# Performance work log

Measured on AMD Instinct MI355X. Metric: run time of the kernel, lower is better.

## Reference

```python
import jax, jax.numpy as jnp
import numpy as np

N_NODES = 100000
N_EDGES = 1200000
MAX_ATOM_TYPE = 100
NUM_FEATURES = 92
GC_DIM = 64          # pre_layer_dim == gc_dim == CGConv channels
NUM_RBF = 32
NUM_GC_LAYERS = 4
CUTOFF_UPPER = 5.0
BN_EPS = 1e-5


def setup_inputs() -> dict:
    key = jax.random.key(0)
    ks = jax.random.split(key, 12)
    atom_types = jax.random.randint(ks[0], (N_NODES,), 0, MAX_ATOM_TYPE, dtype=jnp.int32)
    pos = jax.random.uniform(ks[1], (N_NODES, 3), dtype=jnp.float32) * 6.0  # box side 6 -> many dists < cutoff
    edge_index = jax.random.randint(ks[2], (2, N_EDGES), 0, N_NODES, dtype=jnp.int32)
    # parameters
    emb = jax.random.normal(ks[3], (MAX_ATOM_TYPE, NUM_FEATURES), dtype=jnp.float32)
    s = 1.0 / np.sqrt(NUM_FEATURES)
    pre_W = jax.random.uniform(ks[4], (NUM_FEATURES, GC_DIM), minval=-s, maxval=s, dtype=jnp.float32)
    pre_b = jnp.zeros((GC_DIM,), jnp.float32)
    zdim = 2 * GC_DIM + NUM_RBF  # [x_i, x_j, edge_attr]
    sz = 1.0 / np.sqrt(zdim)
    Wf = jax.random.uniform(ks[5], (NUM_GC_LAYERS, zdim, GC_DIM), minval=-sz, maxval=sz, dtype=jnp.float32)
    bf = jnp.zeros((NUM_GC_LAYERS, GC_DIM), jnp.float32)
    Ws = jax.random.uniform(ks[6], (NUM_GC_LAYERS, zdim, GC_DIM), minval=-sz, maxval=sz, dtype=jnp.float32)
    bs = jnp.zeros((NUM_GC_LAYERS, GC_DIM), jnp.float32)
    bn_gamma = jnp.ones((NUM_GC_LAYERS, GC_DIM), jnp.float32)
    bn_beta = jnp.zeros((NUM_GC_LAYERS, GC_DIM), jnp.float32)
    # ExpNormalSmearing (torchmd-net) init
    start = np.exp(-CUTOFF_UPPER)
    means = jnp.asarray(np.linspace(start, 1.0, NUM_RBF), jnp.float32)
    betas = jnp.full((NUM_RBF,), (2.0 / NUM_RBF * (1.0 - start)) ** -2, jnp.float32)
    return {"atom_types": atom_types, "pos": pos, "edge_index": edge_index,
            "emb": emb, "pre_W": pre_W, "pre_b": pre_b,
            "Wf": Wf, "bf": bf, "Ws": Ws, "bs": bs,
            "bn_gamma": bn_gamma, "bn_beta": bn_beta,
            "means": means, "betas": betas}


def _forward(atom_types, pos, edge_index, emb, pre_W, pre_b, Wf, bf, Ws, bs,
             bn_gamma, bn_beta, means, betas):
    src, dst = edge_index[0], edge_index[1]
    # distance (edge_vec = pos[src] - pos[dst])
    vec = pos[src] - pos[dst]                                  # [E,3]
    dist = jnp.sqrt(jnp.sum(vec * vec, axis=-1) + 1e-12)       # [E]
    # expnorm RBF with cosine cutoff (cutoff_lower = 0)
    cutoff = 0.5 * (jnp.cos(dist * (np.pi / CUTOFF_UPPER)) + 1.0) * (dist < CUTOFF_UPPER)
    alpha = 5.0 / CUTOFF_UPPER
    edge_attr = cutoff[:, None] * jnp.exp(
        -betas * (jnp.exp(-alpha * dist)[:, None] - means) ** 2)  # [E,NUM_RBF]
    # embedding + pre layer
    x = emb[atom_types]                                        # [N,F]
    x = jax.nn.relu(x @ pre_W + pre_b)                         # [N,C]
    # mean-aggregation degree (scatter-mean denominator)
    deg = jax.ops.segment_sum(jnp.ones_like(dist), dst, num_segments=N_NODES)
    inv_deg = jnp.where(deg > 0, 1.0 / jnp.maximum(deg, 1.0), 0.0)[:, None]
    for l in range(NUM_GC_LAYERS):
        # CGConv: z = [x_i, x_j, e]; out = x + mean_j(sigmoid(lin_f(z)) * softplus(lin_s(z)))
        z = jnp.concatenate([x[dst], x[src], edge_attr], axis=-1)   # [E, 2C+R]
        msg = jax.nn.sigmoid(z @ Wf[l] + bf[l]) * jax.nn.softplus(z @ Ws[l] + bs[l])
        agg = jax.ops.segment_sum(msg, dst, num_segments=N_NODES) * inv_deg
        x = x + agg
        # BatchNorm1d (batch statistics, biased var, as in torch training mode)
        mu = jnp.mean(x, axis=0)
        var = jnp.mean((x - mu) ** 2, axis=0)
        x = (x - mu) * jax.lax.rsqrt(var + BN_EPS) * bn_gamma[l] + bn_beta[l]
    return x


def reference(atom_types, pos, edge_index, emb, pre_W, pre_b, Wf, bf, Ws, bs,
              bn_gamma, bn_beta, means, betas):
    return _forward(atom_types, pos, edge_index, emb, pre_W, pre_b, Wf, bf, Ws, bs,
                    bn_gamma, bn_beta, means, betas)
```

## Files before the change

### kernel.cpp

```cpp
#include <hip/hip_runtime.h>
#include <math.h>

#define N_NODES 100000
#define N_EDGES 1200000
#define GC 64
#define RBF 32
#define NLAYERS 4
#define NF 92
#define NATOM 100
#define BN_EPS 1e-5f
#define TILE_GRID 2048
#define NWIN (N_EDGES / 16)
#define LOG2E 1.44269504f
#define LN2 0.69314718f

typedef _Float16 half8 __attribute__((ext_vector_type(8)));
typedef _Float16 half4 __attribute__((ext_vector_type(4)));
typedef _Float16 half2v __attribute__((ext_vector_type(2)));
typedef float f32x4 __attribute__((ext_vector_type(4)));
union U32H2 { unsigned int u; half2v h; };

__global__ __launch_bounds__(256) void deg_kernel(
    const int* __restrict__ ei, int* __restrict__ deg)
{
    int e = blockIdx.x * 256 + threadIdx.x;
    if (e >= N_EDGES) return;
    atomicAdd(&deg[ei[N_EDGES + e]], 1);
}

__global__ __launch_bounds__(256) void scan_a_kernel(const int* __restrict__ deg, int* __restrict__ bsums)
{
    __shared__ int sm[256];
    int tid = threadIdx.x;
    int i = blockIdx.x * 256 + tid;
    int v = (i < N_NODES) ? deg[i] : 0;
    sm[tid] = v;
    __syncthreads();
    for (int s = 128; s > 0; s >>= 1) {
        if (tid < s) sm[tid] += sm[tid + s];
        __syncthreads();
    }
    if (tid == 0) bsums[blockIdx.x] = sm[0];
}

__global__ __launch_bounds__(512) void scan_b_kernel(const int* __restrict__ bsums, int* __restrict__ boffs)
{
    __shared__ int sm[512];
    int tid = threadIdx.x;
    int v = (tid < 391) ? bsums[tid] : 0;
    sm[tid] = v;
    __syncthreads();
    for (int off = 1; off < 512; off <<= 1) {
        int t = (tid >= off) ? sm[tid - off] : 0;
        __syncthreads();
        sm[tid] += t;
        __syncthreads();
    }
    boffs[tid] = (tid == 0) ? 0 : sm[tid - 1];
}

__global__ __launch_bounds__(256) void scan_c_kernel(
    const int* __restrict__ deg, const int* __restrict__ boffs,
    int* __restrict__ row_st, float* __restrict__ inv_deg)
{
    __shared__ int sm[256];
    int tid = threadIdx.x;
    int i = blockIdx.x * 256 + tid;
    int v = (i < N_NODES) ? deg[i] : 0;
    sm[tid] = v;
    __syncthreads();
    for (int off = 1; off < 256; off <<= 1) {
        int t = (tid >= off) ? sm[tid - off] : 0;
        __syncthreads();
        sm[tid] += t;
        __syncthreads();
    }
    if (i <= N_NODES) row_st[i] = boffs[blockIdx.x] + sm[tid] - v;
    if (i < N_NODES) inv_deg[i] = (v > 0) ? (1.0f / (float)v) : 0.0f;
}

__global__ __launch_bounds__(256) void scatter_perm_kernel(
    const int* __restrict__ ei, const int* __restrict__ row_st,
    int* __restrict__ cursor, int2* __restrict__ csr_sd)
{
    int e = blockIdx.x * 256 + threadIdx.x;
    if (e >= N_EDGES) return;
    int s = ei[e];
    int d = ei[N_EDGES + e];
    int p = atomicAdd(&cursor[d], 1);
    csr_sd[row_st[d] + p] = make_int2(s, d);
}

__global__ __launch_bounds__(256) void edge_post_kernel(
    const int2* __restrict__ csr_sd, const float* __restrict__ pos,
    const float* __restrict__ inv_deg,
    const float* __restrict__ means, const float* __restrict__ betas,
    int* __restrict__ csr_src, int* __restrict__ csr_dst,
    unsigned int* __restrict__ ea,
    unsigned char* __restrict__ seg8, int* __restrict__ wnode,
    _Float16* __restrict__ inv_e)
{
    __shared__ int sdst[256];
    int t = blockIdx.x * 256 + threadIdx.x;
    if (t < N_EDGES) {
        int2 v = csr_sd[t];
        int s = v.x, d = v.y;
        csr_src[t] = s;
        csr_dst[t] = d;
        sdst[threadIdx.x] = d;
        inv_e[t] = (_Float16)(inv_deg[d] * LN2);

        float dx = pos[s * 3 + 0] - pos[d * 3 + 0];
        float dy = pos[s * 3 + 1] - pos[d * 3 + 1];
        float dz = pos[s * 3 + 2] - pos[d * 3 + 2];
        float dist = sqrtf(dx * dx + dy * dy + dz * dz + 1e-12f);
        float cut = 0.0f;
        if (dist < 5.0f) cut = 0.5f * (__cosf(dist * 0.6283185307179586f) + 1.0f);
        float ex = __expf(-dist);
        union { _Float16 h[32]; uint4 u[4]; } pk;
#pragma unroll
        for (int k = 0; k < 32; k++) {
            float vk = ex - means[k];
            pk.h[k] = (_Float16)(cut * __expf(-betas[k] * vk * vk));
        }
        uint4* op = (uint4*)(ea + (size_t)t * 16);
        op[0] = pk.u[0];
        op[1] = pk.u[1];
        op[2] = pk.u[2];
        op[3] = pk.u[3];
    }
    __syncthreads();
    if (threadIdx.x < 16) {
        int w0 = blockIdx.x * 16 + threadIdx.x;
        if ((size_t)w0 * 16 < N_EDGES) {
            int lb = threadIdx.x * 16;
            int gb = w0 * 16;
            int prev = -1, sg = -1;
            for (int k = 0; k < 16; k++) {
                int dd = sdst[lb + k];
                if (dd != prev) { sg++; prev = dd; wnode[gb + sg] = dd; }
                seg8[gb + k] = (unsigned char)sg;
            }
            for (int m = sg + 1; m < 16; m++) wnode[gb + m] = -1;
        }
    }
}

__global__ __launch_bounds__(256) void prep_const_kernel(
    const float* __restrict__ Wf, const float* __restrict__ Ws,
    _Float16* __restrict__ wf16, _Float16* __restrict__ ws16,
    const float* __restrict__ emb, const float* __restrict__ pre_W,
    const float* __restrict__ pre_b, float* __restrict__ T)
{
    int b = blockIdx.x;
    if (b < 160) {
        int i = b * 256 + threadIdx.x;
        int l = i / (160 * GC);
        int r = i - l * 160 * GC;
        int k = r >> 6;
        int col = r & 63;
        size_t o = ((size_t)l * GC + col) * 160 + k;
        wf16[o] = (_Float16)(Wf[i] * LOG2E);
        ws16[o] = (_Float16)(Ws[i] * LOG2E);
    } else {
        int a = (b - 160) * 4 + (threadIdx.x >> 6);
        int c = threadIdx.x & 63;
        if (a < NATOM) {
            float acc = pre_b[c];
            for (int k = 0; k < NF; k++) acc = fmaf(emb[a * NF + k], pre_W[k * GC + c], acc);
            T[a * GC + c] = fmaxf(acc, 0.0f);
        }
    }
}

__global__ __launch_bounds__(256) void xinit_kernel(
    const int* __restrict__ atom_types, const float* __restrict__ T,
    float* __restrict__ x, _Float16* __restrict__ x16)
{
    int i = blockIdx.x * 256 + threadIdx.x;
    int n = i >> 4;
    int a = atom_types[n];
    float4 v = ((const float4*)T)[a * 16 + (i & 15)];
    ((float4*)x)[i] = v;
    half4 h = { (_Float16)v.x, (_Float16)v.y, (_Float16)v.z, (_Float16)v.w };
    ((half4*)x16)[i] = h;
}

static __device__ __forceinline__ void proj_mfma16(
    const _Float16* __restrict__ wf, const _Float16* __restrict__ ws,
    const float* __restrict__ bfv, const float* __restrict__ bsv,
    const half8 Bn[2], int cb, int node, unsigned int* __restrict__ P2u)
{
    const int lane = threadIdx.x & 63;
    const int quad = lane >> 4;
    const int r16 = lane & 15;
    f32x4 accf[2], accs[2];
#pragma unroll
    for (int sub = 0; sub < 2; sub++) {
        accf[sub] = (f32x4){0.f, 0.f, 0.f, 0.f};
        accs[sub] = (f32x4){0.f, 0.f, 0.f, 0.f};
    }
#pragma unroll
    for (int kt = 0; kt < 2; kt++) {
#pragma unroll
        for (int sub = 0; sub < 2; sub++) {
            int chan = cb + sub * 16 + r16;
            half8 a = *(const half8*)(wf + (size_t)chan * 160 + kt * 32 + quad * 8);
            half8 b = *(const half8*)(ws + (size_t)chan * 160 + kt * 32 + quad * 8);
            accf[sub] = __builtin_amdgcn_mfma_f32_16x16x32_f16(a, Bn[kt], accf[sub], 0, 0, 0);
            accs[sub] = __builtin_amdgcn_mfma_f32_16x16x32_f16(b, Bn[kt], accs[sub], 0, 0, 0);
        }
    }
#pragma unroll
    for (int sub = 0; sub < 2; sub++) {
        float4 bf4 = *(const float4*)(bfv + cb + sub * 16 + quad * 4);
        float4 bs4 = *(const float4*)(bsv + cb + sub * 16 + quad * 4);
        half8 h = { (_Float16)(accf[sub][0] + bf4.x * LOG2E), (_Float16)(accs[sub][0] + bs4.x * LOG2E),
                    (_Float16)(accf[sub][1] + bf4.y * LOG2E), (_Float16)(accs[sub][1] + bs4.y * LOG2E),
                    (_Float16)(accf[sub][2] + bf4.z * LOG2E), (_Float16)(accs[sub][2] + bs4.z * LOG2E),
                    (_Float16)(accf[sub][3] + bf4.w * LOG2E), (_Float16)(accs[sub][3] + bs4.w * LOG2E) };
        *(half8*)(P2u + (size_t)node * GC + cb + sub * 16 + quad * 4) = h;
    }
}

__global__ __launch_bounds__(256) void proj_kernel(
    const _Float16* __restrict__ x16,
    const _Float16* __restrict__ wf, const _Float16* __restrict__ ws,
    const float* __restrict__ bfv, const float* __restrict__ bsv,
    unsigned int* __restrict__ P2u)
{
    const int lane = threadIdx.x & 63;
    const int wid = threadIdx.x >> 6;
    const int quad = lane >> 4;
    const int r16 = lane & 15;
    const int wgid = blockIdx.x * 4 + wid;
    const int cb = (wgid & 1) * 32;
    const int nb = (wgid >> 1) * 16;
    half8 Bn[2];
    Bn[0] = *(const half8*)(x16 + (size_t)(nb + r16) * GC + quad * 8);
    Bn[1] = *(const half8*)(x16 + (size_t)(nb + r16) * GC + 32 + quad * 8);
    proj_mfma16(wf, ws, bfv, bsv, Bn, cb, nb + r16, P2u);
}

__global__ __launch_bounds__(256) void bnproj_kernel(
    const float* __restrict__ xn, const float* __restrict__ stats,
    const float* __restrict__ gamma, const float* __restrict__ beta,
    float* __restrict__ xout, _Float16* __restrict__ x16,
    const _Float16* __restrict__ wf, const _Float16* __restrict__ ws,
    const float* __restrict__ bfv, const float* __restrict__ bsv,
    unsigned int* __restrict__ P2u)
{
    __shared__ _Float16 lx[32 * 72];
    const int nb = blockIdx.x * 32;
    const float invN = 1.0f / (float)N_NODES;

#pragma unroll
    for (int rep = 0; rep < 2; rep++) {
        int g = rep * 256 + threadIdx.x;
        int gi = blockIdx.x * 512 + g;
        int node = g >> 4;
        int c4 = (g & 15) * 4;
        float4 v = ((const float4*)xn)[gi];
        float vv[4] = {v.x, v.y, v.z, v.w};
        float o[4];
#pragma unroll
        for (int t = 0; t < 4; t++) {
            int c = c4 + t;
            float mu = stats[c] * invN;
            float var = stats[64 + c] * invN - mu * mu;
            float sc = gamma[c] * rsqrtf(var + BN_EPS);
            o[t] = (vv[t] - mu) * sc + beta[c];
        }
        ((float4*)xout)[gi] = make_float4(o[0], o[1], o[2], o[3]);
        half4 h = { (_Float16)o[0], (_Float16)o[1], (_Float16)o[2], (_Float16)o[3] };
        ((half4*)x16)[gi] = h;
        *(half4*)(lx + node * 72 + c4) = h;
    }
    __syncthreads();

    const int lane = threadIdx.x & 63;
    const int wid = threadIdx.x >> 6;
    const int quad = lane >> 4;
    const int r16 = lane & 15;
    const int cb = (wid & 1) * 32;
    const int tn = (wid >> 1) * 16 + r16;
    half8 Bn[2];
    Bn[0] = *(const half8*)(lx + tn * 72 + quad * 8);
    Bn[1] = *(const half8*)(lx + tn * 72 + 32 + quad * 8);
    proj_mfma16(wf, ws, bfv, bsv, Bn, cb, nb + tn, P2u);
}

static __device__ __forceinline__ void compute_win(
    half8 S0, half8 S1, half8 E, int4 d4, int moff,
    const half8 (&WGF)[3][2], const half8 (&WGS)[3][2],
    int r16, int quad, int cb,
    const unsigned char* __restrict__ seg8, const int* __restrict__ wnode,
    const _Float16* __restrict__ inv_e, const unsigned int* __restrict__ P2u,
    float* __restrict__ x)
{
    unsigned int pv0, pv1, pv2, pv3, pv4, pv5, pv6, pv7;
    {
        const unsigned int* p0 = P2u + (size_t)d4.x * GC + cb + r16;
        const unsigned int* p1 = P2u + (size_t)d4.y * GC + cb + r16;
        const unsigned int* p2 = P2u + (size_t)d4.z * GC + cb + r16;
        const unsigned int* p3 = P2u + (size_t)d4.w * GC + cb + r16;
        pv0 = p0[0];  pv4 = p0[16];
        pv1 = p1[0];  pv5 = p1[16];
        pv2 = p2[0];  pv6 = p2[16];
        pv3 = p3[0];  pv7 = p3[16];
    }
    unsigned int segq = *(const unsigned int*)(seg8 + moff + quad * 4);
    int4 wn4 = *(const int4*)(wnode + moff + quad * 4);
    half4 inv4 = *(const half4*)(inv_e + moff + quad * 4);

    const f32x4 zf = (f32x4){0.0f, 0.0f, 0.0f, 0.0f};
    f32x4 accf[2], accs[2];
    __builtin_amdgcn_s_setprio(1);
#pragma unroll
    for (int ctl = 0; ctl < 2; ctl++) {
        accf[ctl] = __builtin_amdgcn_mfma_f32_16x16x32_f16(S0, WGF[0][ctl], zf, 0, 0, 0);
        accs[ctl] = __builtin_amdgcn_mfma_f32_16x16x32_f16(S0, WGS[0][ctl], zf, 0, 0, 0);
        accf[ctl] = __builtin_amdgcn_mfma_f32_16x16x32_f16(S1, WGF[1][ctl], accf[ctl], 0, 0, 0);
        accs[ctl] = __builtin_amdgcn_mfma_f32_16x16x32_f16(S1, WGS[1][ctl], accs[ctl], 0, 0, 0);
        accf[ctl] = __builtin_amdgcn_mfma_f32_16x16x32_f16(E,  WGF[2][ctl], accf[ctl], 0, 0, 0);
        accs[ctl] = __builtin_amdgcn_mfma_f32_16x16x32_f16(E,  WGS[2][ctl], accs[ctl], 0, 0, 0);
    }
    __builtin_amdgcn_s_setprio(0);

    unsigned int pvv[8] = {pv0, pv1, pv2, pv3, pv4, pv5, pv6, pv7};
    half4 msgh[2];
#pragma unroll
    for (int ctl = 0; ctl < 2; ctl++) {
#pragma unroll
        for (int rr = 0; rr < 4; rr++) {
            U32H2 t; t.u = pvv[ctl * 4 + rr];
            float af = accf[ctl][rr] + (float)t.h.x;
            float as = accs[ctl][rr] + (float)t.h.y;
            float sg = __builtin_amdgcn_rcpf(1.0f + __builtin_amdgcn_exp2f(-af));
            float sp = __builtin_amdgcn_logf(1.0f + __builtin_amdgcn_exp2f(as));
            msgh[ctl][rr] = (_Float16)(sg * sp);
        }
    }
    half4 am;
#pragma unroll
    for (int j = 0; j < 4; j++) {
        int sj = (segq >> (8 * j)) & 0xff;
        am[j] = (sj == r16) ? inv4[j] : (_Float16)0.0f;
    }
    int wa[4] = { wn4.x, wn4.y, wn4.z, wn4.w };
#pragma unroll
    for (int ctl = 0; ctl < 2; ctl++) {
        f32x4 red = __builtin_amdgcn_mfma_f32_16x16x16f16(am, msgh[ctl], zf, 0, 0, 0);
#pragma unroll
        for (int rr = 0; rr < 4; rr++) {
            int nd = wa[rr];
            if (nd >= 0) atomicAdd(&x[(size_t)nd * GC + cb + ctl * 16 + r16], red[rr]);
        }
    }
}

#define LOADSET(S0_, S1_, EE_, SRC_, WW_)                                            \
    S0_ = *(const half8*)(x16 + (size_t)(SRC_) * GC + quad * 8);                     \
    S1_ = *(const half8*)(x16 + (size_t)(SRC_) * GC + 32 + quad * 8);                \
    EE_ = *(const half8*)(ea + ((size_t)(WW_) * 16 + r16) * RBF + quad * 8);

__global__ __launch_bounds__(256, 3) void win_mfma_kernel(
    const _Float16* __restrict__ x16, const _Float16* __restrict__ ea,
    const int* __restrict__ csr_src, const int* __restrict__ csr_dst,
    const unsigned char* __restrict__ seg8, const int* __restrict__ wnode,
    const _Float16* __restrict__ inv_e, const unsigned int* __restrict__ P2u,
    const _Float16* __restrict__ wf16, const _Float16* __restrict__ ws16,
    float* __restrict__ x)
{
    const int lane = threadIdx.x & 63;
    const int wid = __builtin_amdgcn_readfirstlane(threadIdx.x >> 6);
    const int quad = lane >> 4;
    const int r16 = lane & 15;
    const int wgid = blockIdx.x * 4 + wid;
    const int cb = (wgid & 1) * 32;
    int w = wgid >> 1;
    const int NSEQ = TILE_GRID * 2;

    half8 WGF[3][2], WGS[3][2];
#pragma unroll
    for (int ctl = 0; ctl < 2; ctl++) {
        const _Float16* wfp = wf16 + (size_t)(cb + ctl * 16 + r16) * 160 + 64 + quad * 8;
        const _Float16* wsp = ws16 + (size_t)(cb + ctl * 16 + r16) * 160 + 64 + quad * 8;
#pragma unroll
        for (int kt = 0; kt < 3; kt++) {
            WGF[kt][ctl] = *(const half8*)(wfp + kt * 32);
            WGS[kt][ctl] = *(const half8*)(wsp + kt * 32);
        }
    }

    int sA = csr_src[w * 16 + r16];
    int4 d4A = *(const int4*)(csr_dst + w * 16 + quad * 4);
    half8 AS0, AS1, AE;
    LOADSET(AS0, AS1, AE, sA, w);
    int moffA = w * 16;

    int wB = w + NSEQ; if (wB >= NWIN) wB = NWIN - 1;
    int sB = csr_src[wB * 16 + r16];
    int4 d4B = *(const int4*)(csr_dst + wB * 16 + quad * 4);
    half8 BS0, BS1, BE;
    LOADSET(BS0, BS1, BE, sB, wB);
    int moffB = wB * 16;

    int wC = wB + NSEQ; if (wC >= NWIN) wC = NWIN - 1;
    int sC = csr_src[wC * 16 + r16];
    int4 d4C = *(const int4*)(csr_dst + wC * 16 + quad * 4);

    while (true) {
        compute_win(AS0, AS1, AE, d4A, moffA,
                    WGF, WGS, r16, quad, cb, seg8, wnode, inv_e, P2u, x);
        LOADSET(AS0, AS1, AE, sC, wC);
        d4A = d4C; moffA = wC * 16;
        wC += NSEQ; if (wC >= NWIN) wC = NWIN - 1;
        sC = csr_src[wC * 16 + r16];
        d4C = *(const int4*)(csr_dst + wC * 16 + quad * 4);
        w += NSEQ;
        if (w >= NWIN) break;

        compute_win(BS0, BS1, BE, d4B, moffB,
                    WGF, WGS, r16, quad, cb, seg8, wnode, inv_e, P2u, x);
        LOADSET(BS0, BS1, BE, sC, wC);
        d4B = d4C; moffB = wC * 16;
        wC += NSEQ; if (wC >= NWIN) wC = NWIN - 1;
        sC = csr_src[wC * 16 + r16];
        d4C = *(const int4*)(csr_dst + wC * 16 + quad * 4);
        w += NSEQ;
        if (w >= NWIN) break;
    }
}

__global__ __launch_bounds__(256) void stats_kernel(const float* __restrict__ x, float* __restrict__ stats)
{
    const int lane = threadIdx.x & 63;
    const int wid = threadIdx.x >> 6;
    int w = blockIdx.x * 4 + wid;
    float s1 = 0.0f, s2 = 0.0f;
    for (int n = w; n < N_NODES; n += 2048) {
        float v = x[(size_t)n * GC + lane];
        s1 += v;
        s2 = fmaf(v, v, s2);
    }
    __shared__ float rs1[4][64];
    __shared__ float rs2[4][64];
    rs1[wid][lane] = s1;
    rs2[wid][lane] = s2;
    __syncthreads();
    if (threadIdx.x < 64) {
        atomicAdd(&stats[lane], rs1[0][lane] + rs1[1][lane] + rs1[2][lane] + rs1[3][lane]);
    } else if (threadIdx.x < 128) {
        int c = threadIdx.x & 63;
        atomicAdd(&stats[64 + c], rs2[0][c] + rs2[1][c] + rs2[2][c] + rs2[3][c]);
    }
}

__global__ __launch_bounds__(256) void bn_kernel(
    const float* __restrict__ xn, const float* __restrict__ stats,
    const float* __restrict__ gamma, const float* __restrict__ beta,
    float* __restrict__ out)
{
    int i = blockIdx.x * 256 + threadIdx.x;
    int c4 = (i & 15) * 4;
    float4 v = ((const float4*)xn)[i];
    float vv[4] = {v.x, v.y, v.z, v.w};
    float o[4];
    const float invN = 1.0f / (float)N_NODES;
#pragma unroll
    for (int t = 0; t < 4; t++) {
        int c = c4 + t;
        float mu = stats[c] * invN;
        float var = stats[64 + c] * invN - mu * mu;
        float sc = gamma[c] * rsqrtf(var + BN_EPS);
        o[t] = (vv[t] - mu) * sc + beta[c];
    }
    ((float4*)out)[i] = make_float4(o[0], o[1], o[2], o[3]);
}

extern "C" void kernel_launch(void* const* d_in, const int* in_sizes, int n_in,
                              void* d_out, int out_size, void* d_ws, size_t ws_size,
                              hipStream_t stream)
{
    const int* atom_types = (const int*)d_in[0];
    const float* pos = (const float*)d_in[1];
    const int* edge_index = (const int*)d_in[2];
    const float* emb = (const float*)d_in[3];
    const float* pre_W = (const float*)d_in[4];
    const float* pre_b = (const float*)d_in[5];
    const float* Wf = (const float*)d_in[6];
    const float* bf = (const float*)d_in[7];
    const float* Ws = (const float*)d_in[8];
    const float* bs = (const float*)d_in[9];
    const float* gamma = (const float*)d_in[10];
    const float* beta = (const float*)d_in[11];
    const float* means = (const float*)d_in[12];
    const float* betas = (const float*)d_in[13];

    char* base = (char*)d_ws;
    char* p = base;
    auto alloc = [&](size_t bytes) -> char* {
        char* r = p;
        p += (bytes + 255) & ~(size_t)255;
        return r;
    };
    unsigned int* ea = (unsigned int*)alloc((size_t)N_EDGES * RBF * 2);
    float* x = (float*)alloc((size_t)N_NODES * GC * 4);
    _Float16* x16 = (_Float16*)alloc((size_t)N_NODES * GC * 2);
    unsigned int* P2u = (unsigned int*)alloc((size_t)N_NODES * GC * 4);
    int2* csr_sd = (int2*)alloc((size_t)N_EDGES * 8);
    int* csr_src = (int*)alloc((size_t)N_EDGES * 4);
    int* csr_dst = (int*)alloc((size_t)N_EDGES * 4);
    int* wnode = (int*)alloc((size_t)N_EDGES * 4);
    unsigned char* seg8 = (unsigned char*)alloc((size_t)N_EDGES);
    _Float16* inv_e = (_Float16*)alloc((size_t)N_EDGES * 2);
    _Float16* wf16 = (_Float16*)alloc((size_t)NLAYERS * GC * 160 * 2);
    _Float16* ws16 = (_Float16*)alloc((size_t)NLAYERS * GC * 160 * 2);
    int* row_st = (int*)alloc((size_t)(N_NODES + 1) * 4);
    float* inv_deg = (float*)alloc((size_t)N_NODES * 4);
    float* T = (float*)alloc((size_t)NATOM * GC * 4);
    int* bsums = (int*)alloc(512 * 4);
    int* boffs = (int*)alloc(512 * 4);
    const size_t ZR_INTS = (size_t)2 * N_NODES + 128 * NLAYERS + 64;
    char* zr = alloc(ZR_INTS * 4);
    int* deg = (int*)zr;
    int* cursor = deg + N_NODES;
    float* stats = (float*)(cursor + N_NODES);

    if ((size_t)(p - base) > ws_size) return;

    (void)hipMemsetAsync(zr, 0, ZR_INTS * 4, stream);

    const int EG = (N_EDGES + 255) / 256;
    deg_kernel<<<EG, 256, 0, stream>>>(edge_index, deg);
    scan_a_kernel<<<391, 256, 0, stream>>>(deg, bsums);
    scan_b_kernel<<<1, 512, 0, stream>>>(bsums, boffs);
    scan_c_kernel<<<391, 256, 0, stream>>>(deg, boffs, row_st, inv_deg);
    scatter_perm_kernel<<<EG, 256, 0, stream>>>(edge_index, row_st, cursor, csr_sd);
    edge_post_kernel<<<EG, 256, 0, stream>>>(csr_sd, pos, inv_deg, means, betas,
                                             csr_src, csr_dst, ea, seg8, wnode, inv_e);
    prep_const_kernel<<<185, 256, 0, stream>>>(Wf, Ws, wf16, ws16, emb, pre_W, pre_b, T);
    xinit_kernel<<<N_NODES * 16 / 256, 256, 0, stream>>>(atom_types, T, x, x16);
    proj_kernel<<<N_NODES / 32, 256, 0, stream>>>(x16, wf16, ws16, bf, bs, P2u);

    for (int l = 0; l < NLAYERS; l++) {
        win_mfma_kernel<<<TILE_GRID, 256, 0, stream>>>(
            x16, (const _Float16*)ea, csr_src, csr_dst, seg8, wnode, inv_e, P2u,
            wf16 + (size_t)l * GC * 160, ws16 + (size_t)l * GC * 160, x);
        stats_kernel<<<512, 256, 0, stream>>>(x, stats + l * 128);
        if (l < NLAYERS - 1) {
            bnproj_kernel<<<N_NODES / 32, 256, 0, stream>>>(
                x, stats + l * 128, gamma + l * GC, beta + l * GC, x, x16,
                wf16 + (size_t)(l + 1) * GC * 160, ws16 + (size_t)(l + 1) * GC * 160,
                bf + (l + 1) * GC, bs + (l + 1) * GC, P2u);
        } else {
            bn_kernel<<<N_NODES * 16 / 256, 256, 0, stream>>>(
                x, stats + l * 128, gamma + l * GC, beta + l * GC, (float*)d_out);
        }
    }
}
```

Baseline: 816.4 us.

## Deepen edge-window prefetch to three buffers and fuse init with projection

The windowed message kernel now keeps three windows of gathered operands in flight instead of two, so global-memory gathers for later windows overlap more compute. Separately, the embedding-lookup init kernel is fused into the first projection kernel through shared memory, removing one launch and a round trip of x16 through global memory. The deeper prefetch raises register pressure, which may lower occupancy or cause spills.

```diff
diff --git a/kernel.cpp b/kernel.cpp
--- a/kernel.cpp
+++ b/kernel.cpp
@@ -173,19 +173,6 @@
     }
 }
 
-__global__ __launch_bounds__(256) void xinit_kernel(
-    const int* __restrict__ atom_types, const float* __restrict__ T,
-    float* __restrict__ x, _Float16* __restrict__ x16)
-{
-    int i = blockIdx.x * 256 + threadIdx.x;
-    int n = i >> 4;
-    int a = atom_types[n];
-    float4 v = ((const float4*)T)[a * 16 + (i & 15)];
-    ((float4*)x)[i] = v;
-    half4 h = { (_Float16)v.x, (_Float16)v.y, (_Float16)v.z, (_Float16)v.w };
-    ((half4*)x16)[i] = h;
-}
-
 static __device__ __forceinline__ void proj_mfma16(
     const _Float16* __restrict__ wf, const _Float16* __restrict__ ws,
     const float* __restrict__ bfv, const float* __restrict__ bsv,
@@ -223,36 +210,15 @@
     }
 }
 
-__global__ __launch_bounds__(256) void proj_kernel(
-    const _Float16* __restrict__ x16,
+__global__ __launch_bounds__(256) void initproj_kernel(
+    const int* __restrict__ atom_types, const float* __restrict__ T,
+    float* __restrict__ x, _Float16* __restrict__ x16,
     const _Float16* __restrict__ wf, const _Float16* __restrict__ ws,
     const float* __restrict__ bfv, const float* __restrict__ bsv,
     unsigned int* __restrict__ P2u)
 {
-    const int lane = threadIdx.x & 63;
-    const int wid = threadIdx.x >> 6;
-    const int quad = lane >> 4;
-    const int r16 = lane & 15;
-    const int wgid = blockIdx.x * 4 + wid;
-    const int cb = (wgid & 1) * 32;
-    const int nb = (wgid >> 1) * 16;
-    half8 Bn[2];
-    Bn[0] = *(const half8*)(x16 + (size_t)(nb + r16) * GC + quad * 8);
-    Bn[1] = *(const half8*)(x16 + (size_t)(nb + r16) * GC + 32 + quad * 8);
-    proj_mfma16(wf, ws, bfv, bsv, Bn, cb, nb + r16, P2u);
-}
-
-__global__ __launch_bounds__(256) void bnproj_kernel(
-    const float* __restrict__ xn, const float* __restrict__ stats,
-    const float* __restrict__ gamma, const float* __restrict__ beta,
-    float* __restrict__ xout, _Float16* __restrict__ x16,
-    const _Float16* __restrict__ wf, const _Float16* __restrict__ ws,
-    const float* __restrict__ bfv, const float* __restrict__ bsv,
-    unsigned int* __restrict__ P2u)
-{
     __shared__ _Float16 lx[32 * 72];
     const int nb = blockIdx.x * 32;
-    const float invN = 1.0f / (float)N_NODES;
 
 #pragma unroll
     for (int rep = 0; rep < 2; rep++) {
@@ -260,19 +226,10 @@
         int gi = blockIdx.x * 512 + g;
         int node = g >> 4;
         int c4 = (g & 15) * 4;
-        float4 v = ((const float4*)xn)[gi];
-        float vv[4] = {v.x, v.y, v.z, v.w};
-        float o[4];
-#pragma unroll
-        for (int t = 0; t < 4; t++) {
-            int c = c4 + t;
-            float mu = stats[c] * invN;
-            float var = stats[64 + c] * invN - mu * mu;
-            float sc = gamma[c] * rsqrtf(var + BN_EPS);
-            o[t] = (vv[t] - mu) * sc + beta[c];
-        }
-        ((float4*)xout)[gi] = make_float4(o[0], o[1], o[2], o[3]);
-        half4 h = { (_Float16)o[0], (_Float16)o[1], (_Float16)o[2], (_Float16)o[3] };
+        int a = atom_types[nb + node];
+        float4 v = ((const float4*)T)[a * 16 + (g & 15)];
+        ((float4*)x)[gi] = v;
+        half4 h = { (_Float16)v.x, (_Float16)v.y, (_Float16)v.z, (_Float16)v.w };
         ((half4*)x16)[gi] = h;
         *(half4*)(lx + node * 72 + c4) = h;
     }
@@ -290,6 +247,54 @@
     proj_mfma16(wf, ws, bfv, bsv, Bn, cb, nb + tn, P2u);
 }
 
+__global__ __launch_bounds__(256) void bnproj_kernel(
+    const float* __restrict__ xn, const float* __restrict__ stats,
+    const float* __restrict__ gamma, const float* __restrict__ beta,
+    float* __restrict__ xout, _Float16* __restrict__ x16,
+    const _Float16* __restrict__ wf, const _Float16* __restrict__ ws,
+    const float* __restrict__ bfv, const float* __restrict__ bsv,
+    unsigned int* __restrict__ P2u)
+{
+    __shared__ _Float16 lx[32 * 72];
+    const int nb = blockIdx.x * 32;
+    const float invN = 1.0f / (float)N_NODES;
+
+#pragma unroll
+    for (int rep = 0; rep < 2; rep++) {
+        int g = rep * 256 + threadIdx.x;
+        int gi = blockIdx.x * 512 + g;
+        int node = g >> 4;
+        int c4 = (g & 15) * 4;
+        float4 v = ((const float4*)xn)[gi];
+        float vv[4] = {v.x, v.y, v.z, v.w};
+        float o[4];
+#pragma unroll
+        for (int t = 0; t < 4; t++) {
+            int c = c4 + t;
+            float mu = stats[c] * invN;
+            float var = stats[64 + c] * invN - mu * mu;
+            float sc = gamma[c] * rsqrtf(var + BN_EPS);
+            o[t] = (vv[t] - mu) * sc + beta[c];
+        }
+        ((float4*)xout)[gi] = make_float4(o[0], o[1], o[2], o[3]);
+        half4 h = { (_Float16)o[0], (_Float16)o[1], (_Float16)o[2], (_Float16)o[3] };
+        ((half4*)x16)[gi] = h;
+        *(half4*)(lx + node * 72 + c4) = h;
+    }
+    __syncthreads();
+
+    const int lane = threadIdx.x & 63;
+    const int wid = threadIdx.x >> 6;
+    const int quad = lane >> 4;
+    const int r16 = lane & 15;
+    const int cb = (wid & 1) * 32;
+    const int tn = (wid >> 1) * 16 + r16;
+    half8 Bn[2];
+    Bn[0] = *(const half8*)(lx + tn * 72 + quad * 8);
+    Bn[1] = *(const half8*)(lx + tn * 72 + 32 + quad * 8);
+    proj_mfma16(wf, ws, bfv, bsv, Bn, cb, nb + tn, P2u);
+}
+
 static __device__ __forceinline__ void compute_win(
     half8 S0, half8 S1, half8 E, int4 d4, int moff,
     const half8 (&WGF)[3][2], const half8 (&WGS)[3][2],
@@ -393,41 +398,61 @@
         }
     }
 
-    int sA = csr_src[w * 16 + r16];
-    int4 d4A = *(const int4*)(csr_dst + w * 16 + quad * 4);
-    half8 AS0, AS1, AE;
-    LOADSET(AS0, AS1, AE, sA, w);
-    int moffA = w * 16;
-
-    int wB = w + NSEQ; if (wB >= NWIN) wB = NWIN - 1;
-    int sB = csr_src[wB * 16 + r16];
-    int4 d4B = *(const int4*)(csr_dst + wB * 16 + quad * 4);
-    half8 BS0, BS1, BE;
-    LOADSET(BS0, BS1, BE, sB, wB);
-    int moffB = wB * 16;
-
-    int wC = wB + NSEQ; if (wC >= NWIN) wC = NWIN - 1;
-    int sC = csr_src[wC * 16 + r16];
-    int4 d4C = *(const int4*)(csr_dst + wC * 16 + quad * 4);
+    half8 AS0, AS1, AE, BS0, BS1, BE, CS0, CS1, CE;
+    int4 d4A, d4B, d4C;
+    int moffA, moffB, moffC;
+    {
+        int s_ = csr_src[w * 16 + r16];
+        d4A = *(const int4*)(csr_dst + w * 16 + quad * 4);
+        LOADSET(AS0, AS1, AE, s_, w);
+        moffA = w * 16;
+    }
+    {
+        int wB = w + NSEQ; if (wB >= NWIN) wB = NWIN - 1;
+        int s_ = csr_src[wB * 16 + r16];
+        d4B = *(const int4*)(csr_dst + wB * 16 + quad * 4);
+        LOADSET(BS0, BS1, BE, s_, wB);
+        moffB = wB * 16;
+    }
+    {
+        int wCx = w + 2 * NSEQ; if (wCx >= NWIN) wCx = NWIN - 1;
+        int s_ = csr_src[wCx * 16 + r16];
+        d4C = *(const int4*)(csr_dst + wCx * 16 + quad * 4);
+        LOADSET(CS0, CS1, CE, s_, wCx);
+        moffC = wCx * 16;
+    }
+    int wD = w + 3 * NSEQ; if (wD >= NWIN) wD = NWIN - 1;
+    int sD = csr_src[wD * 16 + r16];
+    int4 d4D = *(const int4*)(csr_dst + wD * 16 + quad * 4);
 
     while (true) {
         compute_win(AS0, AS1, AE, d4A, moffA,
                     WGF, WGS, r16, quad, cb, seg8, wnode, inv_e, P2u, x);
-        LOADSET(AS0, AS1, AE, sC, wC);
-        d4A = d4C; moffA = wC * 16;
-        wC += NSEQ; if (wC >= NWIN) wC = NWIN - 1;
-        sC = csr_src[wC * 16 + r16];
-        d4C = *(const int4*)(csr_dst + wC * 16 + quad * 4);
+        LOADSET(AS0, AS1, AE, sD, wD);
+        d4A = d4D; moffA = wD * 16;
+        wD += NSEQ; if (wD >= NWIN) wD = NWIN - 1;
+        sD = csr_src[wD * 16 + r16];
+        d4D = *(const int4*)(csr_dst + wD * 16 + quad * 4);
         w += NSEQ;
         if (w >= NWIN) break;
 
         compute_win(BS0, BS1, BE, d4B, moffB,
                     WGF, WGS, r16, quad, cb, seg8, wnode, inv_e, P2u, x);
-        LOADSET(BS0, BS1, BE, sC, wC);
-        d4B = d4C; moffB = wC * 16;
-        wC += NSEQ; if (wC >= NWIN) wC = NWIN - 1;
-        sC = csr_src[wC * 16 + r16];
-        d4C = *(const int4*)(csr_dst + wC * 16 + quad * 4);
+        LOADSET(BS0, BS1, BE, sD, wD);
+        d4B = d4D; moffB = wD * 16;
+        wD += NSEQ; if (wD >= NWIN) wD = NWIN - 1;
+        sD = csr_src[wD * 16 + r16];
+        d4D = *(const int4*)(csr_dst + wD * 16 + quad * 4);
+        w += NSEQ;
+        if (w >= NWIN) break;
+
+        compute_win(CS0, CS1, CE, d4C, moffC,
+                    WGF, WGS, r16, quad, cb, seg8, wnode, inv_e, P2u, x);
+        LOADSET(CS0, CS1, CE, sD, wD);
+        d4C = d4D; moffC = wD * 16;
+        wD += NSEQ; if (wD >= NWIN) wD = NWIN - 1;
+        sD = csr_src[wD * 16 + r16];
+        d4D = *(const int4*)(csr_dst + wD * 16 + quad * 4);
         w += NSEQ;
         if (w >= NWIN) break;
     }
@@ -541,8 +566,8 @@
     edge_post_kernel<<<EG, 256, 0, stream>>>(csr_sd, pos, inv_deg, means, betas,
                                              csr_src, csr_dst, ea, seg8, wnode, inv_e);
     prep_const_kernel<<<185, 256, 0, stream>>>(Wf, Ws, wf16, ws16, emb, pre_W, pre_b, T);
-    xinit_kernel<<<N_NODES * 16 / 256, 256, 0, stream>>>(atom_types, T, x, x16);
-    proj_kernel<<<N_NODES / 32, 256, 0, stream>>>(x16, wf16, ws16, bf, bs, P2u);
+    initproj_kernel<<<N_NODES / 32, 256, 0, stream>>>(atom_types, T, x, x16,
+                                                      wf16, ws16, bf, bs, P2u);
 
     for (int l = 0; l < NLAYERS; l++) {
         win_mfma_kernel<<<TILE_GRID, 256, 0, stream>>>(
```

Measured after the change: 801.0 us. No clear change (-1.9%).
